# Kernel tuning notes

Hardware: AMD Instinct MI355X
Metric: run time of the kernel (lower is better)

## Reference

```python
import jax, jax.numpy as jnp
import numpy as np

D_MODEL = 512; NHEAD = 8; HEAD = D_MODEL // NHEAD
DFF = 2048; K = 31; T = 512; B = 16
EPS = float(np.exp(0.25))  # BasicNorm eps stored in log space, init 0.25


def setup_inputs():
    key = jax.random.key(0)
    ks = jax.random.split(key, 24)
    def rn(k, shape, scale):
        return jax.random.normal(k, shape, jnp.float32) * scale
    si = 1.0 / np.sqrt(D_MODEL); sf = 1.0 / np.sqrt(DFF); sk = 1.0 / np.sqrt(K)
    return {
        "src": jax.random.normal(ks[0], (T, B, D_MODEL), jnp.float32),
        "pos_emb": jax.random.normal(ks[1], (1, 2 * T - 1, D_MODEL), jnp.float32),
        "ffm_w1": rn(ks[2], (DFF, D_MODEL), si), "ffm_b1": jnp.zeros((DFF,), jnp.float32),
        "ffm_w2": rn(ks[3], (D_MODEL, DFF), 0.25 * sf), "ffm_b2": jnp.zeros((D_MODEL,), jnp.float32),
        "ff_w1": rn(ks[4], (DFF, D_MODEL), si), "ff_b1": jnp.zeros((DFF,), jnp.float32),
        "ff_w2": rn(ks[5], (D_MODEL, DFF), 0.25 * sf), "ff_b2": jnp.zeros((D_MODEL,), jnp.float32),
        "in_proj_w": rn(ks[6], (3 * D_MODEL, D_MODEL), si), "in_proj_b": jnp.zeros((3 * D_MODEL,), jnp.float32),
        "out_proj_w": rn(ks[7], (D_MODEL, D_MODEL), 0.25 * si), "out_proj_b": jnp.zeros((D_MODEL,), jnp.float32),
        "linear_pos_w": rn(ks[8], (D_MODEL, D_MODEL), si),
        "pos_bias_u": rn(ks[9], (NHEAD, HEAD), 0.01),
        "pos_bias_v": rn(ks[10], (NHEAD, HEAD), 0.01),
        "conv_pw1_w": rn(ks[11], (2 * D_MODEL, D_MODEL), si), "conv_pw1_b": jnp.zeros((2 * D_MODEL,), jnp.float32),
        "conv_dw_w": rn(ks[12], (D_MODEL, K), sk), "conv_dw_b": jnp.zeros((D_MODEL,), jnp.float32),
        "conv_pw2_w": rn(ks[13], (D_MODEL, D_MODEL), 0.25 * si), "conv_pw2_b": jnp.zeros((D_MODEL,), jnp.float32),
    }


def _double_swish(x):
    return x * jax.nn.sigmoid(x - 1.0)


def _rel_shift(x):
    # x: (B, H, T, 2T-1) -> (B, H, T, T); out[..., i, j] = x[..., i, T-1-i+j]
    t = x.shape[2]
    idx = (t - 1) - jnp.arange(t)[:, None] + jnp.arange(t)[None, :]
    return jnp.take_along_axis(x, idx[None, None], axis=-1)


def reference(src, pos_emb, ffm_w1, ffm_b1, ffm_w2, ffm_b2, ff_w1, ff_b1, ff_w2, ff_b2,
              in_proj_w, in_proj_b, out_proj_w, out_proj_b, linear_pos_w, pos_bias_u, pos_bias_v,
              conv_pw1_w, conv_pw1_b, conv_dw_w, conv_dw_b, conv_pw2_w, conv_pw2_b):
    t, b, c = src.shape
    h, d = pos_bias_u.shape

    def ffw(x, w1, b1, w2, b2):  # ScaledLinear -> DoubleSwish -> ScaledLinear
        return _double_swish(x @ w1.T + b1) @ w2.T + b2

    # macaron feed-forward (ActivationBalancer/Dropout are identity in fwd/eval)
    x = src + ffw(src, ffm_w1, ffm_b1, ffm_w2, ffm_b2)

    # rel-pos self-attention
    qkv = x @ in_proj_w.T + in_proj_b  # (T,B,3C)
    q, k, v = jnp.split(qkv, 3, axis=-1)
    q = (q * (d ** -0.5)).reshape(t, b, h, d).transpose(1, 2, 0, 3)  # (B,H,T,d)
    k = k.reshape(t, b, h, d).transpose(1, 2, 0, 3)
    v = v.reshape(t, b, h, d).transpose(1, 2, 0, 3)
    p = (pos_emb @ linear_pos_w.T).reshape(-1, 2 * t - 1, h, d)[0].transpose(1, 0, 2)  # (H,2T-1,d)
    ac = jnp.einsum('bhtd,bhsd->bhts', q + pos_bias_u[None, :, None, :], k)
    bd = _rel_shift(jnp.einsum('bhtd,hpd->bhtp', q + pos_bias_v[None, :, None, :], p))
    attn = jax.nn.softmax(ac + bd, axis=-1)
    ao = jnp.einsum('bhts,bhsd->bhtd', attn, v).transpose(2, 0, 1, 3).reshape(t, b, c)
    x = x + (ao @ out_proj_w.T + out_proj_b)

    # causal convolution module
    xc = x.transpose(1, 2, 0)  # (B,C,T)
    xc = jnp.einsum('oc,bct->bot', conv_pw1_w, xc) + conv_pw1_b[None, :, None]  # (B,2C,T)
    a, g = jnp.split(xc, 2, axis=1)
    xc = a * jax.nn.sigmoid(g)  # GLU over channel dim
    xc = jnp.pad(xc, ((0, 0), (0, 0), (K - 1, 0)))  # zero cache = causal left pad
    xc = jax.lax.conv_general_dilated(xc, conv_dw_w[:, None, :], (1,), 'VALID',
                                      dimension_numbers=('NCH', 'OIH', 'NCH'),
                                      feature_group_count=c) + conv_dw_b[None, :, None]
    xc = _double_swish(xc)
    xc = jnp.einsum('oc,bct->bot', conv_pw2_w, xc) + conv_pw2_b[None, :, None]
    x = x + xc.transpose(2, 0, 1)

    # second feed-forward
    x = x + ffw(x, ff_w1, ff_b1, ff_w2, ff_b2)

    # BasicNorm over channel dim (balancer is identity in forward)
    x = x * jax.lax.rsqrt(jnp.mean(x * x, axis=-1, keepdims=True) + EPS)
    return x
```

## Files before the change

kernel.cpp:

```cpp
#include <hip/hip_runtime.h>
#include <math.h>

#define T_SEQ 512
#define B_SZ  16
#define C_DIM 512
#define NH    8
#define HD    64
#define DFF_  2048
#define NROWS (T_SEQ * B_SZ)
#define EPS_BN 1.2840254166877414f

typedef unsigned short u16;
typedef __attribute__((ext_vector_type(8))) short bf16x8;
typedef __attribute__((ext_vector_type(4))) float f32x4;

__device__ __forceinline__ float sigmoidf_(float x) { return 1.f / (1.f + __expf(-x)); }
__device__ __forceinline__ float dswishf_(float x)  { return x * sigmoidf_(x - 1.f); }
__device__ __forceinline__ float clampd_(float x)   { return fminf(fmaxf(x, -1e4f), 1e4f); }
__device__ __forceinline__ u16 f2bf_(float x) {
    unsigned u = __float_as_uint(x);
    return (u16)((u + 0x7fffu + ((u >> 16) & 1u)) >> 16);
}
__device__ __forceinline__ float bf2f_(u16 u) {
    return __uint_as_float(((unsigned)u) << 16);
}

template <int ACT, bool HAS_RES, bool O32, bool O16>
__global__ __launch_bounds__(512) void gemm_mfma(
    const u16* __restrict__ A, const u16* __restrict__ W,
    const float* __restrict__ bias, const float* __restrict__ res,
    float* __restrict__ out32, u16* __restrict__ out16, int N, int K, int M)
{
    __shared__ __align__(16) u16 As[2][128 * 32];
    __shared__ __align__(16) u16 Bs[2][128 * 32];
    const int tid  = threadIdx.x;
    const int wv   = tid >> 6;
    const int lane = tid & 63;
    const int wm   = wv >> 2, wn = wv & 3;
    const int m0 = blockIdx.x * 128;
    const int n0 = blockIdx.y * 128;

    const int sc_ = tid & 3;
    const int sr_ = tid >> 2;
    const u16* gA = A + (size_t)(n0 + sr_) * K + sc_ * 8;
    const u16* gB = W + (size_t)(m0 + sr_) * K + sc_ * 8;
    const int ls = sr_ * 32 + sc_ * 8;

    f32x4 acc[4][2];
#pragma unroll
    for (int i = 0; i < 4; ++i)
#pragma unroll
        for (int j = 0; j < 2; ++j) acc[i][j] = (f32x4)0.f;

    const int frow = (lane & 15);
    const int fk   = (lane >> 4) * 8;

    uint4 ra = *(const uint4*)(gA);
    uint4 rb = *(const uint4*)(gB);
    *(uint4*)&As[0][ls] = ra;
    *(uint4*)&Bs[0][ls] = rb;
    __syncthreads();

    int buf = 0;
    for (int k0 = 0; k0 < K; k0 += 32) {
        const bool last = (k0 + 32 >= K);
        if (!last) {
            ra = *(const uint4*)(gA + k0 + 32);
            rb = *(const uint4*)(gB + k0 + 32);
        }
        bf16x8 af[4], bf[2];
#pragma unroll
        for (int i = 0; i < 4; ++i)
            af[i] = *(const bf16x8*)&As[buf][(wm * 64 + i * 16 + frow) * 32 + fk];
#pragma unroll
        for (int j = 0; j < 2; ++j)
            bf[j] = *(const bf16x8*)&Bs[buf][(wn * 32 + j * 16 + frow) * 32 + fk];
#pragma unroll
        for (int i = 0; i < 4; ++i)
#pragma unroll
            for (int j = 0; j < 2; ++j)
                acc[i][j] = __builtin_amdgcn_mfma_f32_16x16x32_bf16(af[i], bf[j], acc[i][j], 0, 0, 0);
        if (!last) {
            const int nb = buf ^ 1;
            *(uint4*)&As[nb][ls] = ra;
            *(uint4*)&Bs[nb][ls] = rb;
            __syncthreads();
            buf = nb;
        }
    }

    const int quad = lane >> 4;
#pragma unroll
    for (int i = 0; i < 4; ++i) {
        const int row = n0 + wm * 64 + i * 16 + quad * 4;
#pragma unroll
        for (int j = 0; j < 2; ++j) {
            const int col = m0 + wn * 32 + j * 16 + (lane & 15);
            const float bv = bias ? bias[col] : 0.f;
#pragma unroll
            for (int r = 0; r < 4; ++r) {
                float v = acc[i][j][r] + bv;
                if (ACT == 1) v = dswishf_(v);
                if (HAS_RES) v += res[(size_t)(row + r) * M + col];
                v = clampd_(v);
                if (O32) out32[(size_t)(row + r) * M + col] = v;
                if (O16) out16[(size_t)(row + r) * M + col] = f2bf_(v);
            }
        }
    }
}

template <int EPI>
__global__ __launch_bounds__(512) void gemm_fused(
    const u16* __restrict__ A, const u16* __restrict__ W,
    const float* __restrict__ bias, const float* __restrict__ ub, const float* __restrict__ vb,
    u16* __restrict__ o_qu, u16* __restrict__ o_qv, u16* __restrict__ o_k,
    u16* __restrict__ o_v, u16* __restrict__ o_p, int N, int K, int M)
{
    __shared__ __align__(16) u16 As[2][128 * 32];
    __shared__ __align__(16) u16 Bs[2][128 * 32];
    const int tid  = threadIdx.x;
    const int wv   = tid >> 6;
    const int lane = tid & 63;
    const int wm   = wv >> 2, wn = wv & 3;
    const int m0 = blockIdx.x * 128;
    const int n0 = blockIdx.y * 128;

    const int sc_ = tid & 3;
    const int sr_ = tid >> 2;
    const u16* gA = A + (size_t)(n0 + sr_) * K + sc_ * 8;
    const u16* gB = W + (size_t)(m0 + sr_) * K + sc_ * 8;
    const int ls = sr_ * 32 + sc_ * 8;

    f32x4 acc[4][2];
#pragma unroll
    for (int i = 0; i < 4; ++i)
#pragma unroll
        for (int j = 0; j < 2; ++j) acc[i][j] = (f32x4)0.f;

    const int frow = (lane & 15);
    const int fk   = (lane >> 4) * 8;

    uint4 ra = *(const uint4*)(gA);
    uint4 rb = *(const uint4*)(gB);
    *(uint4*)&As[0][ls] = ra;
    *(uint4*)&Bs[0][ls] = rb;
    __syncthreads();

    int buf = 0;
    for (int k0 = 0; k0 < K; k0 += 32) {
        const bool last = (k0 + 32 >= K);
        if (!last) {
            ra = *(const uint4*)(gA + k0 + 32);
            rb = *(const uint4*)(gB + k0 + 32);
        }
        bf16x8 af[4], bf[2];
#pragma unroll
        for (int i = 0; i < 4; ++i)
            af[i] = *(const bf16x8*)&As[buf][(wm * 64 + i * 16 + frow) * 32 + fk];
#pragma unroll
        for (int j = 0; j < 2; ++j)
            bf[j] = *(const bf16x8*)&Bs[buf][(wn * 32 + j * 16 + frow) * 32 + fk];
#pragma unroll
        for (int i = 0; i < 4; ++i)
#pragma unroll
            for (int j = 0; j < 2; ++j)
                acc[i][j] = __builtin_amdgcn_mfma_f32_16x16x32_bf16(af[i], bf[j], acc[i][j], 0, 0, 0);
        if (!last) {
            const int nb = buf ^ 1;
            *(uint4*)&As[nb][ls] = ra;
            *(uint4*)&Bs[nb][ls] = rb;
            __syncthreads();
            buf = nb;
        }
    }

    const int quad = lane >> 4;
#pragma unroll
    for (int i = 0; i < 4; ++i) {
        const int rowb = n0 + wm * 64 + i * 16 + quad * 4;
#pragma unroll
        for (int j = 0; j < 2; ++j) {
            const int col = m0 + wn * 32 + j * 16 + (lane & 15);
            if (EPI == 0) {
                const float bv = bias[col];
                const int c = col & 511, h = c >> 6, d = c & 63;
#pragma unroll
                for (int r = 0; r < 4; ++r) {
                    const int row = rowb + r;
                    const float v = clampd_(acc[i][j][r] + bv);
                    const int t = row >> 4, b = row & 15;
                    const size_t dst = ((size_t)(b * 8 + h) * 512 + t) * 64 + d;
                    if (col < 512) {
                        o_qu[dst] = f2bf_(v * 0.125f + ub[c]);
                        o_qv[dst] = f2bf_(v * 0.125f + vb[c]);
                    } else if (col < 1024) {
                        o_k[dst] = f2bf_(v);
                    } else {
                        o_v[dst] = f2bf_(v);
                    }
                }
            } else {
                const int h = col >> 6, d = col & 63;
#pragma unroll
                for (int r = 0; r < 4; ++r)
                    o_p[(size_t)h * 65536 + (size_t)(rowb + r) * 64 + d] = f2bf_(acc[i][j][r]);
            }
        }
    }
}

__global__ __launch_bounds__(512) void gemm_glu_k(
    const u16* __restrict__ A, const u16* __restrict__ W,
    const float* __restrict__ bias, u16* __restrict__ out)
{
    __shared__ __align__(16) u16 As[2][128 * 32];
    __shared__ __align__(16) u16 Ba[2][128 * 32];
    __shared__ __align__(16) u16 Bg[2][128 * 32];
    const int tid  = threadIdx.x;
    const int wv   = tid >> 6;
    const int lane = tid & 63;
    const int wm   = wv >> 2, wn = wv & 3;
    const int m0 = blockIdx.x * 128;
    const int n0 = blockIdx.y * 128;
    const int K = 512;

    const int sc_ = tid & 3;
    const int sr_ = tid >> 2;
    const u16* gA  = A + (size_t)(n0 + sr_) * K + sc_ * 8;
    const u16* gBa = W + (size_t)(m0 + sr_) * K + sc_ * 8;
    const u16* gBg = W + (size_t)(m0 + 512 + sr_) * K + sc_ * 8;
    const int ls = sr_ * 32 + sc_ * 8;

    f32x4 aa[4][2], ag[4][2];
#pragma unroll
    for (int i = 0; i < 4; ++i)
#pragma unroll
        for (int j = 0; j < 2; ++j) { aa[i][j] = (f32x4)0.f; ag[i][j] = (f32x4)0.f; }

    const int frow = (lane & 15);
    const int fk   = (lane >> 4) * 8;

    uint4 ra  = *(const uint4*)(gA);
    uint4 rba = *(const uint4*)(gBa);
    uint4 rbg = *(const uint4*)(gBg);
    *(uint4*)&As[0][ls] = ra;
    *(uint4*)&Ba[0][ls] = rba;
    *(uint4*)&Bg[0][ls] = rbg;
    __syncthreads();

    int buf = 0;
    for (int k0 = 0; k0 < K; k0 += 32) {
        const bool last = (k0 + 32 >= K);
        if (!last) {
            ra  = *(const uint4*)(gA + k0 + 32);
            rba = *(const uint4*)(gBa + k0 + 32);
            rbg = *(const uint4*)(gBg + k0 + 32);
        }
        bf16x8 af[4], bfa[2], bfg[2];
#pragma unroll
        for (int i = 0; i < 4; ++i)
            af[i] = *(const bf16x8*)&As[buf][(wm * 64 + i * 16 + frow) * 32 + fk];
#pragma unroll
        for (int j = 0; j < 2; ++j) {
            bfa[j] = *(const bf16x8*)&Ba[buf][(wn * 32 + j * 16 + frow) * 32 + fk];
            bfg[j] = *(const bf16x8*)&Bg[buf][(wn * 32 + j * 16 + frow) * 32 + fk];
        }
#pragma unroll
        for (int i = 0; i < 4; ++i)
#pragma unroll
            for (int j = 0; j < 2; ++j) {
                aa[i][j] = __builtin_amdgcn_mfma_f32_16x16x32_bf16(af[i], bfa[j], aa[i][j], 0, 0, 0);
                ag[i][j] = __builtin_amdgcn_mfma_f32_16x16x32_bf16(af[i], bfg[j], ag[i][j], 0, 0, 0);
            }
        if (!last) {
            const int nb = buf ^ 1;
            *(uint4*)&As[nb][ls] = ra;
            *(uint4*)&Ba[nb][ls] = rba;
            *(uint4*)&Bg[nb][ls] = rbg;
            __syncthreads();
            buf = nb;
        }
    }

    const int quad = lane >> 4;
#pragma unroll
    for (int i = 0; i < 4; ++i) {
        const int row = n0 + wm * 64 + i * 16 + quad * 4;
#pragma unroll
        for (int j = 0; j < 2; ++j) {
            const int col = m0 + wn * 32 + j * 16 + (lane & 15);
            const float ba = bias[col];
            const float bg = bias[col + 512];
#pragma unroll
            for (int r = 0; r < 4; ++r) {
                const float a = clampd_(aa[i][j][r] + ba);
                const float g = clampd_(ag[i][j][r] + bg);
                out[(size_t)(row + r) * 512 + col] = f2bf_(a * sigmoidf_(g));
            }
        }
    }
}

__device__ __forceinline__ void store_bf4_(u16* out, float4 v) {
    const unsigned lo = (unsigned)f2bf_(v.x) | ((unsigned)f2bf_(v.y) << 16);
    const unsigned hi = (unsigned)f2bf_(v.z) | ((unsigned)f2bf_(v.w) << 16);
    *(uint2*)out = make_uint2(lo, hi);
}

struct WPtrs { const float* p[9]; };
__global__ __launch_bounds__(256) void prep_k(
    WPtrs wp, const float* __restrict__ src, const float* __restrict__ pos,
    const float* __restrict__ cdw,
    u16* __restrict__ wb, u16* __restrict__ src_b, u16* __restrict__ pos_b,
    float* __restrict__ wTd)
{
    const int e = (blockIdx.x * 256 + threadIdx.x) * 4;
    if (e < 6291456) {
        static const int off[10] = {0, 1048576, 2097152, 3145728, 4194304,
                                    4980736, 5242880, 5505024, 6029312, 6291456};
        int r = 0;
#pragma unroll
        for (int k = 1; k < 9; ++k) r += (e >= off[k]);
        store_bf4_(wb + e, *(const float4*)(wp.p[r] + (e - off[r])));
    } else if (e < 6291456 + 4194304) {
        const int e2 = e - 6291456;
        store_bf4_(src_b + e2, *(const float4*)(src + e2));
    } else if (e < 6291456 + 4194304 + 524288) {
        const int e2 = e - (6291456 + 4194304);
        float4 v = make_float4(0.f, 0.f, 0.f, 0.f);
        if (e2 < 1023 * 512) v = *(const float4*)(pos + e2);
        store_bf4_(pos_b + e2, v);
    } else {
        const int e2 = e - (6291456 + 4194304 + 524288);
        if (e2 < 15872) {
#pragma unroll
            for (int q = 0; q < 4; ++q) {
                const int i2 = e2 + q;
                const int j = i2 >> 9, c = i2 & 511;
                wTd[i2] = cdw[c * 31 + j];
            }
        }
    }
}

__global__ __launch_bounds__(256) void vt_k(const u16* __restrict__ in, u16* __restrict__ out)
{
    __shared__ u16 tile[64][65];
    const int s0 = blockIdx.x * 64;
    const int gbh = blockIdx.y;
    const u16* src = in + (size_t)gbh * 512 * 64;
    u16* dst = out + (size_t)gbh * 64 * 512;
    const int tid = threadIdx.x;
#pragma unroll
    for (int q = 0; q < 2; ++q) {
        const int lin = tid * 2 + q;
        const int srow = lin >> 3, c8 = (lin & 7) * 8;
        const uint4 v = *(const uint4*)(src + (size_t)(s0 + srow) * 64 + c8);
        const u16* vu = (const u16*)&v;
#pragma unroll
        for (int e = 0; e < 8; ++e) tile[srow][c8 + e] = vu[e];
    }
    __syncthreads();
#pragma unroll
    for (int q = 0; q < 2; ++q) {
        const int lin = tid * 2 + q;
        const int d = lin >> 3, sc8 = (lin & 7) * 8;
        u16 o[8];
#pragma unroll
        for (int e = 0; e < 8; ++e) o[e] = tile[sc8 + e][d];
        *(uint4*)(dst + (size_t)d * 512 + s0 + sc8) = *(uint4*)o;
    }
}

#define C2S 88
#define PS  72
__global__ __launch_bounds__(256, 4) void flash_attn(
    const u16* __restrict__ qu_b, const u16* __restrict__ qv_b,
    const u16* __restrict__ k_b, const u16* __restrict__ vt_b,
    const u16* __restrict__ p_b, u16* __restrict__ aob)
{
    __shared__ __align__(16) u16 C2ld[4][16 * C2S];
    __shared__ __align__(16) u16 Pld[4][16 * PS];
    const int tid = threadIdx.x;
    const int wv = tid >> 6;
    const int lane = tid & 63;
    const int quad = lane >> 4, ln = lane & 15;
    const int gbh = blockIdx.y;
    const int b = gbh >> 3, h = gbh & 7;
    const int t0 = blockIdx.x * 64 + wv * 16;

    const u16* qu = qu_b + (size_t)gbh * 512 * 64;
    const u16* qv = qv_b + (size_t)gbh * 512 * 64;
    const u16* kb = k_b + (size_t)gbh * 512 * 64;
    const u16* vt = vt_b + (size_t)gbh * 64 * 512;
    const u16* pp = p_b + (size_t)h * 1024 * 64;

    bf16x8 aqu[2], aqv[2];
#pragma unroll
    for (int ks = 0; ks < 2; ++ks) {
        aqu[ks] = *(const bf16x8*)(qu + (size_t)(t0 + ln) * 64 + ks * 32 + quad * 8);
        aqv[ks] = *(const bf16x8*)(qv + (size_t)(t0 + ln) * 64 + ks * 32 + quad * 8);
    }

    const short ob = (short)0x3F80;
    const bf16x8 vone = {ob, ob, ob, ob, ob, ob, ob, ob};

    f32x4 O[4];
#pragma unroll
    for (int nb = 0; nb < 4; ++nb) O[nb] = (f32x4)0.f;
    f32x4 Lacc = (f32x4)0.f;
    float m[4];
#pragma unroll
    for (int r = 0; r < 4; ++r) m[r] = -1e30f;

    u16* c2w = &C2ld[wv][0];
    u16* pw  = &Pld[wv][0];

    for (int s0 = 0; s0 < 512; s0 += 64) {
        f32x4 S[4];
#pragma unroll
        for (int nb = 0; nb < 4; ++nb) S[nb] = (f32x4)0.f;
        __builtin_amdgcn_s_setprio(1);
#pragma unroll
        for (int ks = 0; ks < 2; ++ks)
#pragma unroll
            for (int nb = 0; nb < 4; ++nb) {
                const bf16x8 bk = *(const bf16x8*)(kb + (size_t)(s0 + nb * 16 + ln) * 64 + ks * 32 + quad * 8);
                S[nb] = __builtin_amdgcn_mfma_f32_16x16x32_bf16(aqu[ks], bk, S[nb], 0, 0, 0);
            }
        __builtin_amdgcn_s_setprio(0);
        const int jlo = 496 - t0 + s0;
        f32x4 C2[5];
#pragma unroll
        for (int nb = 0; nb < 5; ++nb) C2[nb] = (f32x4)0.f;
        __builtin_amdgcn_s_setprio(1);
#pragma unroll
        for (int ks = 0; ks < 2; ++ks)
#pragma unroll
            for (int nb = 0; nb < 5; ++nb) {
                const bf16x8 bp = *(const bf16x8*)(pp + (size_t)(jlo + nb * 16 + ln) * 64 + ks * 32 + quad * 8);
                C2[nb] = __builtin_amdgcn_mfma_f32_16x16x32_bf16(aqv[ks], bp, C2[nb], 0, 0, 0);
            }
        __builtin_amdgcn_s_setprio(0);
#pragma unroll
        for (int nb = 0; nb < 5; ++nb)
#pragma unroll
            for (int r = 0; r < 4; ++r)
                c2w[(quad * 4 + r) * C2S + nb * 16 + ln] = f2bf_(C2[nb][r]);

        float sv[4][4];
        float rmax[4] = {-1e30f, -1e30f, -1e30f, -1e30f};
#pragma unroll
        for (int nb = 0; nb < 4; ++nb)
#pragma unroll
            for (int r = 0; r < 4; ++r) {
                const int tloc = quad * 4 + r;
                const int col = nb * 16 + ln + 15 - tloc;
                const float bd = bf2f_(c2w[tloc * C2S + col]);
                const float s = clampd_(S[nb][r] + bd);
                sv[nb][r] = s;
                rmax[r] = fmaxf(rmax[r], s);
            }
#pragma unroll
        for (int off = 1; off < 16; off <<= 1)
#pragma unroll
            for (int r = 0; r < 4; ++r)
                rmax[r] = fmaxf(rmax[r], __shfl_xor(rmax[r], off, 64));

        float alpha[4];
#pragma unroll
        for (int r = 0; r < 4; ++r) {
            const float mn = fmaxf(m[r], rmax[r]);
            alpha[r] = __expf(m[r] - mn);
            m[r] = mn;
        }
#pragma unroll
        for (int nb = 0; nb < 4; ++nb)
#pragma unroll
            for (int r = 0; r < 4; ++r) {
                const float p = __expf(sv[nb][r] - m[r]);
                pw[(quad * 4 + r) * PS + nb * 16 + ln] = f2bf_(p);
            }
#pragma unroll
        for (int nb = 0; nb < 4; ++nb)
#pragma unroll
            for (int r = 0; r < 4; ++r) O[nb][r] *= alpha[r];
#pragma unroll
        for (int r = 0; r < 4; ++r) Lacc[r] *= alpha[r];

        __builtin_amdgcn_s_setprio(1);
#pragma unroll
        for (int ks = 0; ks < 2; ++ks) {
            const bf16x8 ap = *(const bf16x8*)&pw[ln * PS + ks * 32 + quad * 8];
#pragma unroll
            for (int nb = 0; nb < 4; ++nb) {
                const bf16x8 bv = *(const bf16x8*)(vt + (size_t)(nb * 16 + ln) * 512 + s0 + ks * 32 + quad * 8);
                O[nb] = __builtin_amdgcn_mfma_f32_16x16x32_bf16(ap, bv, O[nb], 0, 0, 0);
            }
            Lacc = __builtin_amdgcn_mfma_f32_16x16x32_bf16(ap, vone, Lacc, 0, 0, 0);
        }
        __builtin_amdgcn_s_setprio(0);
    }

    float inv[4];
#pragma unroll
    for (int r = 0; r < 4; ++r) inv[r] = 1.f / Lacc[r];
#pragma unroll
    for (int nb = 0; nb < 4; ++nb)
#pragma unroll
        for (int r = 0; r < 4; ++r) {
            const int t = t0 + quad * 4 + r;
            const int d = nb * 16 + ln;
            aob[((size_t)t * B_SZ + b) * 512 + h * 64 + d] = f2bf_(O[nb][r] * inv[r]);
        }
}

__global__ __launch_bounds__(256) void dwconv_k(
    const u16* __restrict__ g, const float* __restrict__ wT,
    const float* __restrict__ bb, u16* __restrict__ out)
{
    const int idx = blockIdx.x * 256 + threadIdx.x;
    const int c = idx & 511;
    const int b = (idx >> 9) & 15;
    const int t0 = (idx >> 13) * 8;
    float wr[31];
#pragma unroll
    for (int j = 0; j < 31; ++j) wr[j] = wT[j * 512 + c];
    float win[38];
#pragma unroll
    for (int jj = 0; jj < 38; ++jj) {
        const int tt = t0 - 30 + jj;
        win[jj] = (tt >= 0) ? bf2f_(g[((size_t)tt * B_SZ + b) * 512 + c]) : 0.f;
    }
    const float bias = bb[c];
#pragma unroll
    for (int o = 0; o < 8; ++o) {
        float acc = bias;
#pragma unroll
        for (int j = 0; j < 31; ++j) acc += win[o + j] * wr[j];
        out[((size_t)(t0 + o) * B_SZ + b) * 512 + c] = f2bf_(dswishf_(acc));
    }
}

__global__ __launch_bounds__(256) void norm_k(float* __restrict__ x)
{
    const int row = blockIdx.x * 4 + (threadIdx.x >> 6);
    const int lane = threadIdx.x & 63;
    float* r = x + (size_t)row * 512;
    float v[8];
    float ss = 0.f;
#pragma unroll
    for (int j = 0; j < 8; ++j) { v[j] = r[lane + (j << 6)]; ss += v[j] * v[j]; }
#pragma unroll
    for (int o = 32; o > 0; o >>= 1) ss += __shfl_xor(ss, o, 64);
    const float scale = rsqrtf(ss * (1.f / 512.f) + EPS_BN);
#pragma unroll
    for (int j = 0; j < 8; ++j) r[lane + (j << 6)] = v[j] * scale;
}

extern "C" void kernel_launch(void* const* d_in, const int* in_sizes, int n_in,
                              void* d_out, int out_size, void* d_ws, size_t ws_size,
                              hipStream_t stream)
{
    const float* src   = (const float*)d_in[0];
    const float* pos   = (const float*)d_in[1];
    const float* fm_w1 = (const float*)d_in[2];
    const float* fm_b1 = (const float*)d_in[3];
    const float* fm_w2 = (const float*)d_in[4];
    const float* fm_b2 = (const float*)d_in[5];
    const float* f_w1  = (const float*)d_in[6];
    const float* f_b1  = (const float*)d_in[7];
    const float* f_w2  = (const float*)d_in[8];
    const float* f_b2  = (const float*)d_in[9];
    const float* ipw   = (const float*)d_in[10];
    const float* ipb   = (const float*)d_in[11];
    const float* opw   = (const float*)d_in[12];
    const float* opb   = (const float*)d_in[13];
    const float* lpw   = (const float*)d_in[14];
    const float* pbu   = (const float*)d_in[15];
    const float* pbv   = (const float*)d_in[16];
    const float* cpw1  = (const float*)d_in[17];
    const float* cpb1  = (const float*)d_in[18];
    const float* cdw   = (const float*)d_in[19];
    const float* cdb   = (const float*)d_in[20];
    const float* cpw2  = (const float*)d_in[21];
    const float* cpb2  = (const float*)d_in[22];

    float* x = (float*)d_out;

    char* base = (char*)d_ws;
    u16*   wb    = (u16*)base;   base += 6291456ull * 2;
    u16*   src_b = (u16*)base;   base += 4194304ull * 2;
    u16*   pos_b = (u16*)base;   base += 524288ull * 2;
    u16*   xb    = (u16*)base;   base += 4194304ull * 2;
    u16*   hb    = (u16*)base;   base += 16777216ull * 2;
    u16*   aob   = (u16*)base;   base += 4194304ull * 2;
    u16*   qu_b  = (u16*)base;   base += 4194304ull * 2;
    u16*   qv_b  = (u16*)base;   base += 4194304ull * 2;
    u16*   k_b   = (u16*)base;   base += 4194304ull * 2;
    u16*   v_b   = (u16*)base;   base += 4194304ull * 2;
    u16*   vt_b  = (u16*)base;   base += 4194304ull * 2;
    u16*   p_b   = (u16*)base;   base += 524288ull * 2;
    float* wTd   = (float*)base; base += 15872ull * 4;
    u16*   glu_o = (u16*)base;   base += 4194304ull * 2;

    u16* fm_w1b = wb;
    u16* fm_w2b = wb + 1048576;
    u16* f_w1b  = wb + 2097152;
    u16* f_w2b  = wb + 3145728;
    u16* ipwb   = wb + 4194304;
    u16* opwb   = wb + 4980736;
    u16* lpwb   = wb + 5242880;
    u16* cpw1b  = wb + 5505024;
    u16* cpw2b  = wb + 6029312;

    const dim3 blk(256);
    const dim3 blkg(512);

    WPtrs wp = {{fm_w1, fm_w2, f_w1, f_w2, ipw, opw, lpw, cpw1, cpw2}};
    prep_k<<<dim3(10768), blk, 0, stream>>>(wp, src, pos, cdw, wb, src_b, pos_b, wTd);

    gemm_mfma<1, false, false, true><<<dim3(16, 64), blkg, 0, stream>>>(
        src_b, fm_w1b, fm_b1, nullptr, nullptr, hb, NROWS, 512, DFF_);
    gemm_mfma<0, true, true, true><<<dim3(4, 64), blkg, 0, stream>>>(
        hb, fm_w2b, fm_b2, src, x, xb, NROWS, DFF_, 512);

    gemm_fused<0><<<dim3(12, 64), blkg, 0, stream>>>(
        xb, ipwb, ipb, pbu, pbv, qu_b, qv_b, k_b, v_b, nullptr, NROWS, 512, 1536);
    gemm_fused<1><<<dim3(4, 8), blkg, 0, stream>>>(
        pos_b, lpwb, nullptr, nullptr, nullptr,
        nullptr, nullptr, nullptr, nullptr, p_b, 1024, 512, 512);
    vt_k<<<dim3(8, 128), blk, 0, stream>>>(v_b, vt_b);

    flash_attn<<<dim3(8, 128), blk, 0, stream>>>(qu_b, qv_b, k_b, vt_b, p_b, aob);

    gemm_mfma<0, true, true, true><<<dim3(4, 64), blkg, 0, stream>>>(
        aob, opwb, opb, x, x, xb, NROWS, 512, 512);

    gemm_glu_k<<<dim3(4, 64), blkg, 0, stream>>>(xb, cpw1b, cpb1, glu_o);
    dwconv_k<<<dim3(2048), blk, 0, stream>>>(glu_o, wTd, cdb, hb);
    gemm_mfma<0, true, true, true><<<dim3(4, 64), blkg, 0, stream>>>(
        hb, cpw2b, cpb2, x, x, xb, NROWS, 512, 512);

    gemm_mfma<1, false, false, true><<<dim3(16, 64), blkg, 0, stream>>>(
        xb, f_w1b, f_b1, nullptr, nullptr, hb, NROWS, 512, DFF_);
    gemm_mfma<0, true, true, false><<<dim3(4, 64), blkg, 0, stream>>>(
        hb, f_w2b, f_b2, x, x, nullptr, NROWS, DFF_, 512);

    norm_k<<<dim3(NROWS / 4), blk, 0, stream>>>(x);
}
```

Measured before the change: 483.5 us.

## Write V transposed from QKV GEMM epilogue and shuffle rel-shift in registers

The QKV projection epilogue now writes V directly in (b,h,d,t) layout, so the separate V-transpose kernel and its intermediate buffer are gone. In the attention kernel, the relative-position shift of the positional scores no longer goes through a per-wave LDS round trip with bf16 rounding. It is done with cross-lane shuffles on the fp32 accumulators instead. The trade-offs are strided, uncoalesced scattered stores for V in the GEMM epilogue and extra shuffle instructions in the attention inner loop.

```diff
diff --git a/kernel.cpp b/kernel.cpp
--- a/kernel.cpp
+++ b/kernel.cpp
@@ -190,14 +190,14 @@
                     const int row = rowb + r;
                     const float v = clampd_(acc[i][j][r] + bv);
                     const int t = row >> 4, b = row & 15;
-                    const size_t dst = ((size_t)(b * 8 + h) * 512 + t) * 64 + d;
                     if (col < 512) {
+                        const size_t dst = ((size_t)(b * 8 + h) * 512 + t) * 64 + d;
                         o_qu[dst] = f2bf_(v * 0.125f + ub[c]);
                         o_qv[dst] = f2bf_(v * 0.125f + vb[c]);
                     } else if (col < 1024) {
-                        o_k[dst] = f2bf_(v);
+                        o_k[((size_t)(b * 8 + h) * 512 + t) * 64 + d] = f2bf_(v);
                     } else {
-                        o_v[dst] = f2bf_(v);
+                        o_v[((size_t)(b * 8 + h) * 64 + d) * 512 + t] = f2bf_(v);
                     }
                 }
             } else {
@@ -344,43 +344,12 @@
     }
 }
 
-__global__ __launch_bounds__(256) void vt_k(const u16* __restrict__ in, u16* __restrict__ out)
-{
-    __shared__ u16 tile[64][65];
-    const int s0 = blockIdx.x * 64;
-    const int gbh = blockIdx.y;
-    const u16* src = in + (size_t)gbh * 512 * 64;
-    u16* dst = out + (size_t)gbh * 64 * 512;
-    const int tid = threadIdx.x;
-#pragma unroll
-    for (int q = 0; q < 2; ++q) {
-        const int lin = tid * 2 + q;
-        const int srow = lin >> 3, c8 = (lin & 7) * 8;
-        const uint4 v = *(const uint4*)(src + (size_t)(s0 + srow) * 64 + c8);
-        const u16* vu = (const u16*)&v;
-#pragma unroll
-        for (int e = 0; e < 8; ++e) tile[srow][c8 + e] = vu[e];
-    }
-    __syncthreads();
-#pragma unroll
-    for (int q = 0; q < 2; ++q) {
-        const int lin = tid * 2 + q;
-        const int d = lin >> 3, sc8 = (lin & 7) * 8;
-        u16 o[8];
-#pragma unroll
-        for (int e = 0; e < 8; ++e) o[e] = tile[sc8 + e][d];
-        *(uint4*)(dst + (size_t)d * 512 + s0 + sc8) = *(uint4*)o;
-    }
-}
-
-#define C2S 88
 #define PS  72
 __global__ __launch_bounds__(256, 4) void flash_attn(
     const u16* __restrict__ qu_b, const u16* __restrict__ qv_b,
     const u16* __restrict__ k_b, const u16* __restrict__ vt_b,
     const u16* __restrict__ p_b, u16* __restrict__ aob)
 {
-    __shared__ __align__(16) u16 C2ld[4][16 * C2S];
     __shared__ __align__(16) u16 Pld[4][16 * PS];
     const int tid = threadIdx.x;
     const int wv = tid >> 6;
@@ -414,8 +383,7 @@
 #pragma unroll
     for (int r = 0; r < 4; ++r) m[r] = -1e30f;
 
-    u16* c2w = &C2ld[wv][0];
-    u16* pw  = &Pld[wv][0];
+    u16* pw = &Pld[wv][0];
 
     for (int s0 = 0; s0 < 512; s0 += 64) {
         f32x4 S[4];
@@ -443,25 +411,24 @@
                 C2[nb] = __builtin_amdgcn_mfma_f32_16x16x32_bf16(aqv[ks], bp, C2[nb], 0, 0, 0);
             }
         __builtin_amdgcn_s_setprio(0);
-#pragma unroll
-        for (int nb = 0; nb < 5; ++nb)
-#pragma unroll
-            for (int r = 0; r < 4; ++r)
-                c2w[(quad * 4 + r) * C2S + nb * 16 + ln] = f2bf_(C2[nb][r]);
 
         float sv[4][4];
         float rmax[4] = {-1e30f, -1e30f, -1e30f, -1e30f};
 #pragma unroll
-        for (int nb = 0; nb < 4; ++nb)
-#pragma unroll
-            for (int r = 0; r < 4; ++r) {
-                const int tloc = quad * 4 + r;
-                const int col = nb * 16 + ln + 15 - tloc;
-                const float bd = bf2f_(c2w[tloc * C2S + col]);
+        for (int r = 0; r < 4; ++r) {
+            const int idx  = ln + 15 - quad * 4 - r;
+            const int srcl = (lane & 48) | (idx & 15);
+            float g[5];
+#pragma unroll
+            for (int cb = 0; cb < 5; ++cb) g[cb] = __shfl(C2[cb][r], srcl, 64);
+#pragma unroll
+            for (int nb = 0; nb < 4; ++nb) {
+                const float bd = (idx < 16) ? g[nb] : g[nb + 1];
                 const float s = clampd_(S[nb][r] + bd);
                 sv[nb][r] = s;
                 rmax[r] = fmaxf(rmax[r], s);
             }
+        }
 #pragma unroll
         for (int off = 1; off < 16; off <<= 1)
 #pragma unroll
@@ -599,7 +566,6 @@
     u16*   qu_b  = (u16*)base;   base += 4194304ull * 2;
     u16*   qv_b  = (u16*)base;   base += 4194304ull * 2;
     u16*   k_b   = (u16*)base;   base += 4194304ull * 2;
-    u16*   v_b   = (u16*)base;   base += 4194304ull * 2;
     u16*   vt_b  = (u16*)base;   base += 4194304ull * 2;
     u16*   p_b   = (u16*)base;   base += 524288ull * 2;
     float* wTd   = (float*)base; base += 15872ull * 4;
@@ -627,11 +593,10 @@
         hb, fm_w2b, fm_b2, src, x, xb, NROWS, DFF_, 512);
 
     gemm_fused<0><<<dim3(12, 64), blkg, 0, stream>>>(
-        xb, ipwb, ipb, pbu, pbv, qu_b, qv_b, k_b, v_b, nullptr, NROWS, 512, 1536);
+        xb, ipwb, ipb, pbu, pbv, qu_b, qv_b, k_b, vt_b, nullptr, NROWS, 512, 1536);
     gemm_fused<1><<<dim3(4, 8), blkg, 0, stream>>>(
         pos_b, lpwb, nullptr, nullptr, nullptr,
         nullptr, nullptr, nullptr, nullptr, p_b, 1024, 512, 512);
-    vt_k<<<dim3(8, 128), blk, 0, stream>>>(v_b, vt_b);
 
     flash_attn<<<dim3(8, 128), blk, 0, stream>>>(qu_b, qv_b, k_b, vt_b, p_b, aob);
 
```

Result: slower. 561.9 us (+16.2%).
